# Kernel optimization log

Hardware: AMD Instinct MI355X
Metric: run time of the kernel (lower is better)

## Reference

```python
import jax, jax.numpy as jnp
import numpy as np

EPS = 1e-5

def _graph_conv(x, src, dst, W, b, N):
    # DGL GraphConv, norm='both': D_out^{-1/2} then aggregate then D_in^{-1/2}
    ones = jnp.ones((src.shape[0],), x.dtype)
    out_deg = jnp.clip(jax.ops.segment_sum(ones, src, num_segments=N), 1.0)
    in_deg = jnp.clip(jax.ops.segment_sum(ones, dst, num_segments=N), 1.0)
    h = (x * (out_deg ** -0.5)[:, None]) @ W          # [N, out] (mult W before gather)
    agg = jax.ops.segment_sum(h[src], dst, num_segments=N)  # [N, out] irregular scatter
    return agg * (in_deg ** -0.5)[:, None] + b

def _bn_relu(h, gamma, beta):
    # BatchNorm1d in training mode: batch stats over node axis (biased var)
    mu = jnp.mean(h, axis=0)
    var = jnp.mean((h - mu) ** 2, axis=0)
    return jax.nn.relu((h - mu) * jax.lax.rsqrt(var + EPS) * gamma + beta)

def setup_inputs() -> dict:
    key = jax.random.key(0)
    ks = jax.random.split(key, 6)
    N, E, F, H, C = 100000, 1000000, 128, 128, 16
    return {
        "x": jax.random.normal(ks[0], (N, F), dtype=jnp.float32),
        "src": jax.random.randint(ks[1], (E,), 0, N, dtype=jnp.int32),
        "dst": jax.random.randint(ks[2], (E,), 0, N, dtype=jnp.int32),
        "W1": jax.random.normal(ks[3], (F, H), dtype=jnp.float32) * 0.05,
        "b1": jnp.zeros((H,), jnp.float32),
        "g1": jnp.ones((H,), jnp.float32),
        "be1": jnp.zeros((H,), jnp.float32),
        "W2": jax.random.normal(ks[4], (H, H), dtype=jnp.float32) * 0.05,
        "b2": jnp.zeros((H,), jnp.float32),
        "g2": jnp.ones((H,), jnp.float32),
        "be2": jnp.zeros((H,), jnp.float32),
        "Wc": jax.random.normal(ks[5], (H, C), dtype=jnp.float32) * 0.05,
        "bc": jnp.zeros((C,), jnp.float32),
    }

def reference(x, src, dst, W1, b1, g1, be1, W2, b2, g2, be2, Wc, bc):
    N = x.shape[0]
    h = _bn_relu(_graph_conv(x, src, dst, W1, b1, N), g1, be1)  # dropout = identity (eval)
    h = _bn_relu(_graph_conv(h, src, dst, W2, b2, N), g2, be2)
    return h @ Wc + bc  # [N, num_cls]
```

## Files before the change

### kernel.cpp

```cpp
#include <hip/hip_runtime.h>

#define FDIM 128
#define MAXDEG 64
#define GATHERB 2048
#define NREP 32

#define RSIZE 128
#define RSHIFT 7
#define RCAP 1024
#define CCAP 11776
#define PCAP 96

typedef unsigned short ushort_t;
typedef unsigned int uint_t;
typedef __attribute__((ext_vector_type(8))) short short8;
typedef __attribute__((ext_vector_type(16))) float float16;

__device__ __forceinline__ float bflo(uint_t u) { return __uint_as_float(u << 16); }
__device__ __forceinline__ float bfhi(uint_t u) { return __uint_as_float(u & 0xffff0000u); }
__device__ __forceinline__ ushort_t f2bf(float f) {
    uint_t u = __float_as_uint(f);
    return (ushort_t)((u + 0x7fffu + ((u >> 16) & 1u)) >> 16);
}
__device__ __forceinline__ uint_t pack2bf(float lo, float hi) {
    return (uint_t)f2bf(lo) | ((uint_t)f2bf(hi) << 16);
}

__global__ __launch_bounds__(256) void prep_kernel(
    const float* __restrict__ W1, const float* __restrict__ W2,
    ushort_t* __restrict__ wb1, ushort_t* __restrict__ wb2,
    float* __restrict__ statsR, int nstat) {
    int i0 = blockIdx.x * 256 + threadIdx.x;
    int stride = gridDim.x * 256;
    for (int j = i0; j < nstat; j += stride) statsR[j] = 0.f;
    for (int j = i0; j < FDIM * FDIM; j += stride) {
        int n = j >> 7, k = j & 127;
        wb1[j] = f2bf(W1[k * FDIM + n]);
        wb2[j] = f2bf(W2[k * FDIM + n]);
    }
}

__global__ __launch_bounds__(256) void fused1_kernel(
    const int* __restrict__ src, const int* __restrict__ dst,
    uint_t* __restrict__ bktD, int* __restrict__ baseD,
    uint_t* __restrict__ bktS, int* __restrict__ baseS,
    const ushort_t* __restrict__ wb1,
    const float* __restrict__ x, ushort_t* __restrict__ outb,
    int E, int P, int R, int N, int G1B) {
    __shared__ __align__(16) char smem[52224];
    int t = threadIdx.x;
    int bid = blockIdx.x;

    if (bid >= 2 * P) {
        typedef ushort_t row136[136];
        row136* zt = (row136*)smem;
        row136* wt = (row136*)(smem + 17408);
        int idx = bid - 2 * P;
        if (idx >= G1B) return;
        int base = idx * 64;

        const uint4* wb4 = (const uint4*)wb1;
        for (int i = t; i < FDIM * 16; i += 256) {
            int n = i >> 4, q = i & 15;
            *(uint4*)&wt[n][q * 8] = wb4[n * 16 + q];
        }
        const float4* x4 = (const float4*)x;
        for (int i = t; i < 64 * 32; i += 256) {
            int row = i >> 5, c4 = i & 31;
            int grow = base + row;
            uint2 o = make_uint2(0u, 0u);
            if (grow < N) {
                float4 v = x4[(size_t)grow * 32 + c4];
                o.x = pack2bf(v.x, v.y);
                o.y = pack2bf(v.z, v.w);
            }
            *(uint2*)&zt[row][c4 * 4] = o;
        }
        __syncthreads();

        int wv = t >> 6, lane = t & 63;
        int rt = wv >> 1;
        int m = lane & 31;
        int kg = lane >> 5;

        short8 af[8];
#pragma unroll
        for (int kk = 0; kk < 8; kk++)
            af[kk] = *(const short8*)&zt[rt * 32 + m][kk * 16 + kg * 8];

#pragma unroll
        for (int cc = 0; cc < 2; cc++) {
            int ct = (wv & 1) * 2 + cc;
            float16 acc = {0, 0, 0, 0, 0, 0, 0, 0, 0, 0, 0, 0, 0, 0, 0, 0};
#pragma unroll
            for (int kk = 0; kk < 8; kk++) {
                short8 bf = *(const short8*)&wt[ct * 32 + m][kk * 16 + kg * 8];
                acc = __builtin_amdgcn_mfma_f32_32x32x16_bf16(af[kk], bf, acc, 0, 0, 0);
            }
            int col = ct * 32 + m;
#pragma unroll
            for (int r = 0; r < 16; r++) {
                int row = base + rt * 32 + (r & 3) + 8 * (r >> 2) + 4 * kg;
                if (row < N) outb[(size_t)row * FDIM + col] = f2bf(acc[r]);
            }
        }
        return;
    }

    uint4* buf4 = (uint4*)smem;
    int* hist = (int*)(smem + 47104);
    int* scanbuf = (int*)(smem + 51200);
    uint_t* buf = (uint_t*)buf4;

    int role = bid >= P;
    int p = role ? bid - P : bid;
    const int* key = role ? src : dst;
    int e0 = p * CCAP;
    int e1 = min(E, e0 + CCAP);
    int cnt = e1 - e0;
    int nq = cnt >> 2;

    for (int r = t; r < R; r += 256) hist[r] = 0;
    __syncthreads();
    const int4* key4 = (const int4*)(key + e0);
    for (int i = t; i < nq; i += 256) {
        int4 kv = key4[i];
        atomicAdd(&hist[kv.x >> RSHIFT], 1);
        atomicAdd(&hist[kv.y >> RSHIFT], 1);
        atomicAdd(&hist[kv.z >> RSHIFT], 1);
        atomicAdd(&hist[kv.w >> RSHIFT], 1);
    }
    for (int i = e0 + (nq << 2) + t; i < e1; i += 256) atomicAdd(&hist[key[i] >> RSHIFT], 1);
    __syncthreads();

    int b0 = t * 4;
    int hv[4];
    int s0 = 0;
#pragma unroll
    for (int k = 0; k < 4; k++) {
        hv[k] = (b0 + k < R) ? hist[b0 + k] : 0;
        s0 += hv[k];
    }
    scanbuf[t] = s0;
    __syncthreads();
    for (int off = 1; off < 256; off <<= 1) {
        int v = (t >= off) ? scanbuf[t - off] : 0;
        __syncthreads();
        scanbuf[t] += v;
        __syncthreads();
    }
    int run = scanbuf[t] - s0;
    int* baseG = role ? baseS : baseD;
#pragma unroll
    for (int k = 0; k < 4; k++) {
        if (b0 + k < R) {
            baseG[(b0 + k) * P + p] = run;
            hist[b0 + k] = run;
        }
        run += hv[k];
    }
    if (t == 0) baseG[R * P + p] = cnt;
    __syncthreads();

    const int4* src4 = (const int4*)(src + e0);
    for (int i = t; i < nq; i += 256) {
        int4 kv = key4[i];
        int4 sv = role ? kv : src4[i];
        int s0i = atomicAdd(&hist[kv.x >> RSHIFT], 1);
        buf[s0i] = role ? (uint_t)kv.x : (((uint_t)(kv.x & (RSIZE - 1)) << 25) | (uint_t)sv.x);
        int s1i = atomicAdd(&hist[kv.y >> RSHIFT], 1);
        buf[s1i] = role ? (uint_t)kv.y : (((uint_t)(kv.y & (RSIZE - 1)) << 25) | (uint_t)sv.y);
        int s2i = atomicAdd(&hist[kv.z >> RSHIFT], 1);
        buf[s2i] = role ? (uint_t)kv.z : (((uint_t)(kv.z & (RSIZE - 1)) << 25) | (uint_t)sv.z);
        int s3i = atomicAdd(&hist[kv.w >> RSHIFT], 1);
        buf[s3i] = role ? (uint_t)kv.w : (((uint_t)(kv.w & (RSIZE - 1)) << 25) | (uint_t)sv.w);
    }
    for (int i = e0 + (nq << 2) + t; i < e1; i += 256) {
        int kv = key[i];
        int slot = atomicAdd(&hist[kv >> RSHIFT], 1);
        uint_t entry = role ? (uint_t)kv
                            : (((uint_t)(kv & (RSIZE - 1)) << 25) | (uint_t)src[i]);
        buf[slot] = entry;
    }
    __syncthreads();

    uint_t* outp = role ? bktS : bktD;
    uint4* og = (uint4*)(outp + (size_t)e0);
    int n4 = (cnt + 3) >> 2;
    for (int j = t; j < n4; j += 256) og[j] = buf4[j];
}

__global__ __launch_bounds__(256) void build_kernel(
    const uint_t* __restrict__ bktD, const int* __restrict__ baseD,
    const uint_t* __restrict__ bktS, const int* __restrict__ baseS,
    int* __restrict__ eidx, int* __restrict__ cnt, int* __restrict__ cs,
    ushort_t* __restrict__ hb, int N, int P) {
    __shared__ uint4 ell4[RSIZE][MAXDEG / 4];
    __shared__ int cntN[RSIZE], csN[RSIZE];
    __shared__ float csi[RSIZE];
    __shared__ int dB0[PCAP], dB1[PCAP], sB0[PCAP], sB1[PCAP];
    uint_t* ell = (uint_t*)ell4;
    int t = threadIdx.x;
    int r = blockIdx.x;

    if (t < RSIZE) { cntN[t] = 0; csN[t] = 0; }
    for (int i = t; i < P; i += 256) {
        dB0[i] = baseD[r * P + i];
        dB1[i] = baseD[(r + 1) * P + i];
        sB0[i] = baseS[r * P + i];
        sB1[i] = baseS[(r + 1) * P + i];
    }
    __syncthreads();

    int wave = t >> 6, lane = t & 63;
    for (int p = wave; p < P; p += 4) {
        int b = dB0[p], len = dB1[p] - b;
        const uint_t* seg = bktD + (size_t)p * CCAP + b;
        for (int i = lane; i < len; i += 64) {
            uint_t e = seg[i];
            int dl = e >> 25;
            uint_t s = e & 0x1FFFFFFu;
            int slot = atomicAdd(&cntN[dl], 1);
            if (slot < MAXDEG) ell[dl * MAXDEG + slot] = s;
        }
        int b2 = sB0[p], len2 = sB1[p] - b2;
        const uint_t* seg2 = bktS + (size_t)p * CCAP + b2;
        for (int i = lane; i < len2; i += 64)
            atomicAdd(&csN[seg2[i] & (RSIZE - 1)], 1);
    }
    __syncthreads();

    int base = r * RSIZE;
    for (int i = t; i < RSIZE * (MAXDEG / 4); i += 256) {
        int n = i >> 4, q = i & 15;
        int g = base + n;
        if (g < N && q * 4 < min(cntN[n], MAXDEG))
            ((uint4*)eidx)[(size_t)g * (MAXDEG / 4) + q] = ell4[n][q];
    }
    if (t < RSIZE) {
        int g = base + t;
        csi[t] = rsqrtf((float)max(csN[t], 1));
        if (g < N) { cnt[g] = cntN[t]; cs[g] = csN[t]; }
    }
    __syncthreads();

    uint2* h2 = (uint2*)hb;
    for (int i = t; i < RSIZE * 32; i += 256) {
        int row = i >> 5, cq = i & 31;
        int g = base + row;
        if (g < N) {
            float sc = csi[row];
            uint2 u = h2[(size_t)g * 32 + cq];
            u.x = pack2bf(bflo(u.x) * sc, bfhi(u.x) * sc);
            u.y = pack2bf(bflo(u.y) * sc, bfhi(u.y) * sc);
            h2[(size_t)g * 32 + cq] = u;
        }
    }
}

__global__ __launch_bounds__(256) void gather_kernel(const ushort_t* __restrict__ hb,
                                                     const int* __restrict__ eidx,
                                                     const int* __restrict__ cnt,
                                                     const float* __restrict__ b,
                                                     ushort_t* __restrict__ outb,
                                                     float* __restrict__ statsRep, int N) {
    __shared__ float4 redS[256];
    __shared__ float4 redQ[256];
    int t = threadIdx.x;
    int wave = t >> 6, lane = t & 63;
    int half = lane >> 5, sub = lane & 31;
    const int STRIDE = GATHERB * 4;
    int gw = blockIdx.x * 4 + wave;
    const uint2* h2 = (const uint2*)hb;
    uint2* o2 = (uint2*)outb;
    float4 bb = ((const float4*)b)[sub];
    float st0 = 0, st1 = 0, st2 = 0, st3 = 0, sq0 = 0, sq1 = 0, sq2 = 0, sq3 = 0;

    int node = gw;
    int deg = 0, ridx = 0;
    if (node < N) {
        deg = cnt[node];
        ridx = (lane < 32) ? eidx[(size_t)node * MAXDEG + lane] : 0;
    }
    while (node < N) {
        if (__builtin_expect(deg > 32, 0)) {
            if (lane >= 32) ridx = eidx[(size_t)node * MAXDEG + lane];
        }
        int nnode = node + STRIDE;
        int ndeg = 0, nridx = 0;
        if (nnode < N) {
            ndeg = cnt[nnode];
            nridx = (lane < 32) ? eidx[(size_t)nnode * MAXDEG + lane] : 0;
        }

        int e = min(deg, MAXDEG);
        float a0 = 0, a1 = 0, a2 = 0, a3 = 0;
        float c0 = 0, c1 = 0, c2 = 0, c3 = 0;
        int j = 0;
        for (; j + 7 < e; j += 8) {
            int iA = __shfl(ridx, j + half);
            int iB = __shfl(ridx, j + 2 + half);
            int iC = __shfl(ridx, j + 4 + half);
            int iD = __shfl(ridx, j + 6 + half);
            uint2 uA = h2[(size_t)iA * 32 + sub];
            uint2 uB = h2[(size_t)iB * 32 + sub];
            uint2 uC = h2[(size_t)iC * 32 + sub];
            uint2 uD = h2[(size_t)iD * 32 + sub];
            a0 += bflo(uA.x); a1 += bfhi(uA.x); a2 += bflo(uA.y); a3 += bfhi(uA.y);
            c0 += bflo(uB.x); c1 += bfhi(uB.x); c2 += bflo(uB.y); c3 += bfhi(uB.y);
            a0 += bflo(uC.x); a1 += bfhi(uC.x); a2 += bflo(uC.y); a3 += bfhi(uC.y);
            c0 += bflo(uD.x); c1 += bfhi(uD.x); c2 += bflo(uD.y); c3 += bfhi(uD.y);
        }
        for (; j + 3 < e; j += 4) {
            int iA = __shfl(ridx, j + half);
            int iB = __shfl(ridx, j + 2 + half);
            uint2 uA = h2[(size_t)iA * 32 + sub];
            uint2 uB = h2[(size_t)iB * 32 + sub];
            a0 += bflo(uA.x); a1 += bfhi(uA.x); a2 += bflo(uA.y); a3 += bfhi(uA.y);
            c0 += bflo(uB.x); c1 += bfhi(uB.x); c2 += bflo(uB.y); c3 += bfhi(uB.y);
        }
        for (; j < e; j += 2) {
            int jj = j + half;
            bool take = jj < e;
            int i0 = __shfl(ridx, take ? jj : (e - 1));
            float m = take ? 1.f : 0.f;
            uint2 u = h2[(size_t)i0 * 32 + sub];
            a0 = fmaf(bflo(u.x), m, a0); a1 = fmaf(bfhi(u.x), m, a1);
            a2 = fmaf(bflo(u.y), m, a2); a3 = fmaf(bfhi(u.y), m, a3);
        }
        a0 += c0; a1 += c1; a2 += c2; a3 += c3;
        a0 += __shfl_xor(a0, 32);
        a1 += __shfl_xor(a1, 32);
        a2 += __shfl_xor(a2, 32);
        a3 += __shfl_xor(a3, 32);
        if (half == 0) {
            float isc = rsqrtf((float)max(deg, 1));
            uint2 o;
            o.x = pack2bf(fmaf(a0, isc, bb.x), fmaf(a1, isc, bb.y));
            o.y = pack2bf(fmaf(a2, isc, bb.z), fmaf(a3, isc, bb.w));
            o2[(size_t)node * 32 + sub] = o;
            float v0 = bflo(o.x), v1 = bfhi(o.x), v2 = bflo(o.y), v3 = bfhi(o.y);
            st0 += v0; st1 += v1; st2 += v2; st3 += v3;
            sq0 = fmaf(v0, v0, sq0); sq1 = fmaf(v1, v1, sq1);
            sq2 = fmaf(v2, v2, sq2); sq3 = fmaf(v3, v3, sq3);
        }
        node = nnode; deg = ndeg; ridx = nridx;
    }

    redS[t] = make_float4(st0, st1, st2, st3);
    redQ[t] = make_float4(sq0, sq1, sq2, sq3);
    __syncthreads();
    if (t < 32) {
        float4 s = make_float4(0, 0, 0, 0), q = make_float4(0, 0, 0, 0);
#pragma unroll
        for (int w = 0; w < 4; w++) {
            float4 a = redS[w * 64 + t];
            float4 z = redQ[w * 64 + t];
            s.x += a.x; s.y += a.y; s.z += a.z; s.w += a.w;
            q.x += z.x; q.y += z.y; q.z += z.z; q.w += z.w;
        }
        float* dstp = statsRep + (size_t)(blockIdx.x & (NREP - 1)) * 256;
        atomicAdd(&dstp[t * 4 + 0], s.x);
        atomicAdd(&dstp[t * 4 + 1], s.y);
        atomicAdd(&dstp[t * 4 + 2], s.z);
        atomicAdd(&dstp[t * 4 + 3], s.w);
        atomicAdd(&dstp[128 + t * 4 + 0], q.x);
        atomicAdd(&dstp[128 + t * 4 + 1], q.y);
        atomicAdd(&dstp[128 + t * 4 + 2], q.z);
        atomicAdd(&dstp[128 + t * 4 + 3], q.w);
    }
}

__global__ __launch_bounds__(256) void gemm2_kernel(const ushort_t* __restrict__ hb,
                                                    const ushort_t* __restrict__ wb,
                                                    const int* __restrict__ cs,
                                                    const float* __restrict__ statsRep,
                                                    const float* __restrict__ g,
                                                    const float* __restrict__ be,
                                                    ushort_t* __restrict__ outb, int N,
                                                    float invN) {
    __shared__ ushort_t zt[64][136];
    __shared__ ushort_t wt[128][136];
    __shared__ float Ash[FDIM], Bsh[FDIM];
    int t = threadIdx.x;
    int base = blockIdx.x * 64;

    if (t < FDIM) {
        float s = 0.f, q = 0.f;
        for (int r = 0; r < NREP; r++) {
            s += statsRep[r * 256 + t];
            q += statsRep[r * 256 + 128 + t];
        }
        float mu = s * invN;
        float var = q * invN - mu * mu;
        float a = g[t] * rsqrtf(var + 1e-5f);
        Ash[t] = a;
        Bsh[t] = be[t] - mu * a;
    }
    const uint4* wb4 = (const uint4*)wb;
    for (int i = t; i < FDIM * 16; i += 256) {
        int n = i >> 4, q = i & 15;
        *(uint4*)&wt[n][q * 8] = wb4[n * 16 + q];
    }
    __syncthreads();

    const uint_t* h1 = (const uint_t*)hb;
    for (int i = t; i < 64 * 64; i += 256) {
        int row = i >> 6, cp = i & 63;
        int grow = base + row;
        uint_t o = 0;
        if (grow < N) {
            uint_t u = h1[(size_t)grow * 64 + cp];
            float s = rsqrtf((float)max(cs[grow], 1));
            float v0 = fmaxf(fmaf(bflo(u), Ash[cp * 2], Bsh[cp * 2]), 0.f) * s;
            float v1 = fmaxf(fmaf(bfhi(u), Ash[cp * 2 + 1], Bsh[cp * 2 + 1]), 0.f) * s;
            o = pack2bf(v0, v1);
        }
        *(uint_t*)&zt[row][cp * 2] = o;
    }
    __syncthreads();

    int wv = t >> 6, lane = t & 63;
    int rt = wv >> 1;
    int m = lane & 31;
    int kg = lane >> 5;

    short8 af[8];
#pragma unroll
    for (int kk = 0; kk < 8; kk++)
        af[kk] = *(const short8*)&zt[rt * 32 + m][kk * 16 + kg * 8];

#pragma unroll
    for (int cc = 0; cc < 2; cc++) {
        int ct = (wv & 1) * 2 + cc;
        float16 acc = {0, 0, 0, 0, 0, 0, 0, 0, 0, 0, 0, 0, 0, 0, 0, 0};
#pragma unroll
        for (int kk = 0; kk < 8; kk++) {
            short8 bf = *(const short8*)&wt[ct * 32 + m][kk * 16 + kg * 8];
            acc = __builtin_amdgcn_mfma_f32_32x32x16_bf16(af[kk], bf, acc, 0, 0, 0);
        }
        int col = ct * 32 + m;
#pragma unroll
        for (int r = 0; r < 16; r++) {
            int row = base + rt * 32 + (r & 3) + 8 * (r >> 2) + 4 * kg;
            if (row < N) outb[(size_t)row * FDIM + col] = f2bf(acc[r]);
        }
    }
}

__global__ __launch_bounds__(256) void cls_kernel(const ushort_t* __restrict__ hb,
                                                  const float* __restrict__ Wc,
                                                  const float* __restrict__ bc,
                                                  const float* __restrict__ statsRep,
                                                  const float* __restrict__ g,
                                                  const float* __restrict__ be,
                                                  float* __restrict__ out, int N, float invN) {
    __shared__ float wcl[FDIM * 16];
    __shared__ float red[16][256];
    __shared__ float Ash[FDIM], Bsh[FDIM];
    int t = threadIdx.x;
    int base = blockIdx.x * 64;
#pragma unroll
    for (int i = 0; i < 8; i++) wcl[t + i * 256] = Wc[t + i * 256];
    if (t < FDIM) {
        float s = 0.f, q = 0.f;
        for (int r = 0; r < NREP; r++) {
            s += statsRep[r * 256 + t];
            q += statsRep[r * 256 + 128 + t];
        }
        float mu = s * invN;
        float var = q * invN - mu * mu;
        float a = g[t] * rsqrtf(var + 1e-5f);
        Ash[t] = a;
        Bsh[t] = be[t] - mu * a;
    }
    __syncthreads();

    int node = base + (t >> 2);
    int q4 = t & 3;
    float acc[16];
#pragma unroll
    for (int c = 0; c < 16; c++) acc[c] = 0.f;

    if (node < N) {
        const uint2* hu2 = (const uint2*)((const uint_t*)hb + (size_t)node * 64 + q4 * 16);
        const float* Af = Ash + q4 * 32;
        const float* Bf = Bsh + q4 * 32;
#pragma unroll 1
        for (int kk = 0; kk < 8; kk++) {
            uint2 u = hu2[kk];
            float4 ab = *(const float4*)&Af[kk * 4];
            float4 bb = *(const float4*)&Bf[kk * 4];
            float v0 = fmaxf(fmaf(bflo(u.x), ab.x, bb.x), 0.f);
            float v1 = fmaxf(fmaf(bfhi(u.x), ab.y, bb.y), 0.f);
            float v2 = fmaxf(fmaf(bflo(u.y), ab.z, bb.z), 0.f);
            float v3 = fmaxf(fmaf(bfhi(u.y), ab.w, bb.w), 0.f);
            int k0 = q4 * 32 + kk * 4;
            const float* w0 = &wcl[k0 * 16];
#pragma unroll
            for (int c = 0; c < 16; c++) {
                float s = fmaf(v0, w0[c], fmaf(v1, w0[16 + c], fmaf(v2, w0[32 + c], v3 * w0[48 + c])));
                acc[c] += s;
            }
        }
    }
#pragma unroll
    for (int c = 0; c < 16; c++) red[c][t] = acc[c];
    __syncthreads();
#pragma unroll
    for (int i = t; i < 64 * 16; i += 256) {
        int n = i >> 4, c = i & 15;
        float4 p = *(const float4*)&red[c][n * 4];
        int grow = base + n;
        if (grow < N) out[(size_t)grow * 16 + c] = (p.x + p.y) + (p.z + p.w) + bc[c];
    }
}

extern "C" void kernel_launch(void* const* d_in, const int* in_sizes, int n_in,
                              void* d_out, int out_size, void* d_ws, size_t ws_size,
                              hipStream_t stream) {
    const float* x  = (const float*)d_in[0];
    const int* src  = (const int*)d_in[1];
    const int* dst  = (const int*)d_in[2];
    const float* W1 = (const float*)d_in[3];
    const float* b1 = (const float*)d_in[4];
    const float* g1 = (const float*)d_in[5];
    const float* be1= (const float*)d_in[6];
    const float* W2 = (const float*)d_in[7];
    const float* b2 = (const float*)d_in[8];
    const float* g2 = (const float*)d_in[9];
    const float* be2= (const float*)d_in[10];
    const float* Wc = (const float*)d_in[11];
    const float* bc = (const float*)d_in[12];
    float* out = (float*)d_out;

    int N = in_sizes[0] / FDIM;
    int E = in_sizes[1];
    size_t NB = (size_t)N * FDIM;

    ushort_t* bufA = (ushort_t*)d_ws;
    ushort_t* bufB = bufA + NB;
    int* cs        = (int*)(bufB + NB);
    int* cnt       = cs + N;
    float* statsR1 = (float*)(cnt + N);
    float* statsR2 = statsR1 + NREP * 256;
    int* eidx      = (int*)(statsR2 + NREP * 256);
    ushort_t* wb1  = (ushort_t*)(eidx + (size_t)N * MAXDEG);
    ushort_t* wb2  = wb1 + FDIM * FDIM;

    uint_t* bktD = (uint_t*)bufB;
    uint_t* bktS = bktD + (size_t)PCAP * CCAP;
    int* baseD   = (int*)(bktS + (size_t)PCAP * CCAP);
    int* baseS   = baseD + (RCAP + 1) * PCAP;

    int P = (E + CCAP - 1) / CCAP;
    int R = (N + RSIZE - 1) >> RSHIFT;
    int G1B = (N + 63) / 64;

    prep_kernel<<<64, 256, 0, stream>>>(W1, W2, wb1, wb2, statsR1, 2 * NREP * 256);

    fused1_kernel<<<2 * P + G1B, 256, 0, stream>>>(
        src, dst, bktD, baseD, bktS, baseS, wb1, x, bufA, E, P, R, N, G1B);
    build_kernel<<<R, 256, 0, stream>>>(bktD, baseD, bktS, baseS, eidx, cnt, cs, bufA, N, P);

    float invN = 1.0f / N;

    gather_kernel<<<GATHERB, 256, 0, stream>>>(bufA, eidx, cnt, b1, bufB, statsR1, N);

    gemm2_kernel<<<(N + 63) / 64, 256, 0, stream>>>(bufB, wb2, cs, statsR1, g1, be1, bufA, N, invN);
    gather_kernel<<<GATHERB, 256, 0, stream>>>(bufA, eidx, cnt, b2, bufB, statsR2, N);

    cls_kernel<<<(N + 63) / 64, 256, 0, stream>>>(bufB, Wc, bc, statsR2, g2, be2, out, N, invN);
}
```

Baseline: 316.1 us.

## Widen gather loads to 16-byte rows with 4 edges per wave, shrink ELL width

```diff
diff --git a/kernel.cpp b/kernel.cpp
--- a/kernel.cpp
+++ b/kernel.cpp
@@ -1,7 +1,7 @@
 #include <hip/hip_runtime.h>
 
 #define FDIM 128
-#define MAXDEG 64
+#define MAXDEG 48
 #define GATHERB 2048
 #define NREP 32
 
@@ -232,7 +232,7 @@
 
     int base = r * RSIZE;
     for (int i = t; i < RSIZE * (MAXDEG / 4); i += 256) {
-        int n = i >> 4, q = i & 15;
+        int n = i / (MAXDEG / 4), q = i % (MAXDEG / 4);
         int g = base + n;
         if (g < N && q * 4 < min(cntN[n], MAXDEG))
             ((uint4*)eidx)[(size_t)g * (MAXDEG / 4) + q] = ell4[n][q];
@@ -264,17 +264,19 @@
                                                      const float* __restrict__ b,
                                                      ushort_t* __restrict__ outb,
                                                      float* __restrict__ statsRep, int N) {
-    __shared__ float4 redS[256];
-    __shared__ float4 redQ[256];
+    __shared__ float redS[4 * 128];
+    __shared__ float redQ[4 * 128];
     int t = threadIdx.x;
     int wave = t >> 6, lane = t & 63;
-    int half = lane >> 5, sub = lane & 31;
+    int q4 = lane >> 4;
+    int sub = lane & 15;
     const int STRIDE = GATHERB * 4;
     int gw = blockIdx.x * 4 + wave;
-    const uint2* h2 = (const uint2*)hb;
-    uint2* o2 = (uint2*)outb;
-    float4 bb = ((const float4*)b)[sub];
-    float st0 = 0, st1 = 0, st2 = 0, st3 = 0, sq0 = 0, sq1 = 0, sq2 = 0, sq3 = 0;
+    const uint4* h4 = (const uint4*)hb;
+    uint4* o4 = (uint4*)outb;
+    float4 bb0 = ((const float4*)b)[sub * 2];
+    float4 bb1 = ((const float4*)b)[sub * 2 + 1];
+    float st[8] = {}, sq[8] = {};
 
     int node = gw;
     int deg = 0, ridx = 0;
@@ -284,7 +286,7 @@
     }
     while (node < N) {
         if (__builtin_expect(deg > 32, 0)) {
-            if (lane >= 32) ridx = eidx[(size_t)node * MAXDEG + lane];
+            if (lane >= 32 && lane < MAXDEG) ridx = eidx[(size_t)node * MAXDEG + lane];
         }
         int nnode = node + STRIDE;
         int ndeg = 0, nridx = 0;
@@ -294,80 +296,82 @@
         }
 
         int e = min(deg, MAXDEG);
-        float a0 = 0, a1 = 0, a2 = 0, a3 = 0;
-        float c0 = 0, c1 = 0, c2 = 0, c3 = 0;
+        float a[8] = {0, 0, 0, 0, 0, 0, 0, 0};
+        float c[8] = {0, 0, 0, 0, 0, 0, 0, 0};
         int j = 0;
         for (; j + 7 < e; j += 8) {
-            int iA = __shfl(ridx, j + half);
-            int iB = __shfl(ridx, j + 2 + half);
-            int iC = __shfl(ridx, j + 4 + half);
-            int iD = __shfl(ridx, j + 6 + half);
-            uint2 uA = h2[(size_t)iA * 32 + sub];
-            uint2 uB = h2[(size_t)iB * 32 + sub];
-            uint2 uC = h2[(size_t)iC * 32 + sub];
-            uint2 uD = h2[(size_t)iD * 32 + sub];
-            a0 += bflo(uA.x); a1 += bfhi(uA.x); a2 += bflo(uA.y); a3 += bfhi(uA.y);
-            c0 += bflo(uB.x); c1 += bfhi(uB.x); c2 += bflo(uB.y); c3 += bfhi(uB.y);
-            a0 += bflo(uC.x); a1 += bfhi(uC.x); a2 += bflo(uC.y); a3 += bfhi(uC.y);
-            c0 += bflo(uD.x); c1 += bfhi(uD.x); c2 += bflo(uD.y); c3 += bfhi(uD.y);
+            int iA = __shfl(ridx, j + q4);
+            int iB = __shfl(ridx, j + 4 + q4);
+            uint4 uA = h4[(size_t)iA * 16 + sub];
+            uint4 uB = h4[(size_t)iB * 16 + sub];
+            a[0] += bflo(uA.x); a[1] += bfhi(uA.x); a[2] += bflo(uA.y); a[3] += bfhi(uA.y);
+            a[4] += bflo(uA.z); a[5] += bfhi(uA.z); a[6] += bflo(uA.w); a[7] += bfhi(uA.w);
+            c[0] += bflo(uB.x); c[1] += bfhi(uB.x); c[2] += bflo(uB.y); c[3] += bfhi(uB.y);
+            c[4] += bflo(uB.z); c[5] += bfhi(uB.z); c[6] += bflo(uB.w); c[7] += bfhi(uB.w);
         }
         for (; j + 3 < e; j += 4) {
-            int iA = __shfl(ridx, j + half);
-            int iB = __shfl(ridx, j + 2 + half);
-            uint2 uA = h2[(size_t)iA * 32 + sub];
-            uint2 uB = h2[(size_t)iB * 32 + sub];
-            a0 += bflo(uA.x); a1 += bfhi(uA.x); a2 += bflo(uA.y); a3 += bfhi(uA.y);
-            c0 += bflo(uB.x); c1 += bfhi(uB.x); c2 += bflo(uB.y); c3 += bfhi(uB.y);
-        }
-        for (; j < e; j += 2) {
-            int jj = j + half;
+            int iA = __shfl(ridx, j + q4);
+            uint4 uA = h4[(size_t)iA * 16 + sub];
+            a[0] += bflo(uA.x); a[1] += bfhi(uA.x); a[2] += bflo(uA.y); a[3] += bfhi(uA.y);
+            a[4] += bflo(uA.z); a[5] += bfhi(uA.z); a[6] += bflo(uA.w); a[7] += bfhi(uA.w);
+        }
+        if (j < e) {
+            int jj = j + q4;
             bool take = jj < e;
             int i0 = __shfl(ridx, take ? jj : (e - 1));
             float m = take ? 1.f : 0.f;
-            uint2 u = h2[(size_t)i0 * 32 + sub];
-            a0 = fmaf(bflo(u.x), m, a0); a1 = fmaf(bfhi(u.x), m, a1);
-            a2 = fmaf(bflo(u.y), m, a2); a3 = fmaf(bfhi(u.y), m, a3);
-        }
-        a0 += c0; a1 += c1; a2 += c2; a3 += c3;
-        a0 += __shfl_xor(a0, 32);
-        a1 += __shfl_xor(a1, 32);
-        a2 += __shfl_xor(a2, 32);
-        a3 += __shfl_xor(a3, 32);
-        if (half == 0) {
+            uint4 u = h4[(size_t)i0 * 16 + sub];
+            a[0] = fmaf(bflo(u.x), m, a[0]); a[1] = fmaf(bfhi(u.x), m, a[1]);
+            a[2] = fmaf(bflo(u.y), m, a[2]); a[3] = fmaf(bfhi(u.y), m, a[3]);
+            a[4] = fmaf(bflo(u.z), m, a[4]); a[5] = fmaf(bfhi(u.z), m, a[5]);
+            a[6] = fmaf(bflo(u.w), m, a[6]); a[7] = fmaf(bfhi(u.w), m, a[7]);
+        }
+#pragma unroll
+        for (int k = 0; k < 8; k++) {
+            a[k] += c[k];
+            a[k] += __shfl_xor(a[k], 16);
+            a[k] += __shfl_xor(a[k], 32);
+        }
+        if (q4 == 0) {
             float isc = rsqrtf((float)max(deg, 1));
-            uint2 o;
-            o.x = pack2bf(fmaf(a0, isc, bb.x), fmaf(a1, isc, bb.y));
-            o.y = pack2bf(fmaf(a2, isc, bb.z), fmaf(a3, isc, bb.w));
-            o2[(size_t)node * 32 + sub] = o;
-            float v0 = bflo(o.x), v1 = bfhi(o.x), v2 = bflo(o.y), v3 = bfhi(o.y);
-            st0 += v0; st1 += v1; st2 += v2; st3 += v3;
-            sq0 = fmaf(v0, v0, sq0); sq1 = fmaf(v1, v1, sq1);
-            sq2 = fmaf(v2, v2, sq2); sq3 = fmaf(v3, v3, sq3);
+            float v0 = fmaf(a[0], isc, bb0.x), v1 = fmaf(a[1], isc, bb0.y);
+            float v2 = fmaf(a[2], isc, bb0.z), v3 = fmaf(a[3], isc, bb0.w);
+            float v4 = fmaf(a[4], isc, bb1.x), v5 = fmaf(a[5], isc, bb1.y);
+            float v6 = fmaf(a[6], isc, bb1.z), v7 = fmaf(a[7], isc, bb1.w);
+            uint4 o;
+            o.x = pack2bf(v0, v1); o.y = pack2bf(v2, v3);
+            o.z = pack2bf(v4, v5); o.w = pack2bf(v6, v7);
+            o4[(size_t)node * 16 + sub] = o;
+            float w0 = bflo(o.x), w1 = bfhi(o.x), w2 = bflo(o.y), w3 = bfhi(o.y);
+            float w4 = bflo(o.z), w5 = bfhi(o.z), w6 = bflo(o.w), w7 = bfhi(o.w);
+            st[0] += w0; st[1] += w1; st[2] += w2; st[3] += w3;
+            st[4] += w4; st[5] += w5; st[6] += w6; st[7] += w7;
+            sq[0] = fmaf(w0, w0, sq[0]); sq[1] = fmaf(w1, w1, sq[1]);
+            sq[2] = fmaf(w2, w2, sq[2]); sq[3] = fmaf(w3, w3, sq[3]);
+            sq[4] = fmaf(w4, w4, sq[4]); sq[5] = fmaf(w5, w5, sq[5]);
+            sq[6] = fmaf(w6, w6, sq[6]); sq[7] = fmaf(w7, w7, sq[7]);
         }
         node = nnode; deg = ndeg; ridx = nridx;
     }
 
-    redS[t] = make_float4(st0, st1, st2, st3);
-    redQ[t] = make_float4(sq0, sq1, sq2, sq3);
-    __syncthreads();
-    if (t < 32) {
-        float4 s = make_float4(0, 0, 0, 0), q = make_float4(0, 0, 0, 0);
+    if (q4 == 0) {
+#pragma unroll
+        for (int k = 0; k < 8; k++) {
+            redS[wave * 128 + sub * 8 + k] = st[k];
+            redQ[wave * 128 + sub * 8 + k] = sq[k];
+        }
+    }
+    __syncthreads();
+    if (t < 128) {
+        float s = 0.f, qq = 0.f;
 #pragma unroll
         for (int w = 0; w < 4; w++) {
-            float4 a = redS[w * 64 + t];
-            float4 z = redQ[w * 64 + t];
-            s.x += a.x; s.y += a.y; s.z += a.z; s.w += a.w;
-            q.x += z.x; q.y += z.y; q.z += z.z; q.w += z.w;
+            s += redS[w * 128 + t];
+            qq += redQ[w * 128 + t];
         }
         float* dstp = statsRep + (size_t)(blockIdx.x & (NREP - 1)) * 256;
-        atomicAdd(&dstp[t * 4 + 0], s.x);
-        atomicAdd(&dstp[t * 4 + 1], s.y);
-        atomicAdd(&dstp[t * 4 + 2], s.z);
-        atomicAdd(&dstp[t * 4 + 3], s.w);
-        atomicAdd(&dstp[128 + t * 4 + 0], q.x);
-        atomicAdd(&dstp[128 + t * 4 + 1], q.y);
-        atomicAdd(&dstp[128 + t * 4 + 2], q.z);
-        atomicAdd(&dstp[128 + t * 4 + 3], q.w);
+        atomicAdd(&dstp[t], s);
+        atomicAdd(&dstp[128 + t], qq);
     }
 }
 
```

Result: slower. 332.7 us (+5.3%).
